# Performance work log

Measured on AMD Instinct MI355X. Metric: run time of the kernel, lower is better.

The kernel has to match this reference:

```python
import jax, jax.numpy as jnp
import numpy as np

B = 2048      # env batch (graphs)
A = 8         # agents per graph (fully connected)
N = B * A     # total nodes
DIN = 192     # raw obs dim
HD = 256      # h_dim (base MLP)
MD = 256      # mem_dim (GRU)
GD = 128      # gnn_dim (per-head GATv2 out, concat=False -> head mean)
H = 4         # GAT heads
NA = 20       # n_actions
ED = 3        # edge_dim


def setup_inputs() -> dict:
    key = jax.random.key(0)
    ks = jax.random.split(key, 16)
    # fully-connected directed graph per group of A agents, no self loops
    s, d = np.meshgrid(np.arange(A), np.arange(A), indexing='ij')
    mask = s != d
    s = s[mask]; d = d[mask]                     # [A*(A-1)]
    off = (np.arange(B) * A)[:, None]
    src = (off + s[None, :]).reshape(-1)
    dst = (off + d[None, :]).reshape(-1)
    edge_index = jnp.asarray(np.stack([src, dst]), dtype=jnp.int32)  # [2, E]
    E = src.shape[0]
    p = lambda k, sh: jax.random.normal(ks[k], sh, jnp.float32) * 0.02
    return {
        'inputs': jax.random.normal(ks[0], (N, DIN), jnp.float32),
        'hidden_states': jax.random.normal(ks[1], (N, MD), jnp.float32) * 0.1,
        'edge_index': edge_index,
        'edge_attr': jax.random.uniform(ks[2], (E, ED), jnp.float32),
        # base MLP (2 layers: Linear+ReLU+LayerNorm)
        'W1': p(3, (DIN, HD)), 'b1': jnp.zeros(HD), 'g1': jnp.ones(HD), 'be1': jnp.zeros(HD),
        'W2': p(4, (HD, HD)),  'b2': jnp.zeros(HD), 'g2': jnp.ones(HD), 'be2': jnp.zeros(HD),
        # GRUCell
        'Wih': p(5, (3 * MD, HD)), 'Whh': p(6, (3 * MD, MD)),
        'bih': jnp.zeros(3 * MD), 'bhh': jnp.zeros(3 * MD),
        # GATv2Conv (edge_dim=3, heads=4, concat=False, residual)
        'Wl': p(7, (MD, H * GD)), 'bl': jnp.zeros(H * GD),
        'Wr': p(8, (MD, H * GD)), 'br': jnp.zeros(H * GD),
        'att': p(9, (H, GD)),
        'We': p(10, (ED, H * GD)),
        'Wres': p(11, (MD, GD)),
        'bg': jnp.zeros(GD),
        # head: LayerNorm + Linear
        'lng': jnp.ones(GD), 'lnb': jnp.zeros(GD),
        'Wout': p(12, (GD, NA)), 'bout': jnp.zeros(NA),
    }


def _ln(x, g, b):
    mu = jnp.mean(x, -1, keepdims=True)
    xc = x - mu
    v = jnp.mean(xc * xc, -1, keepdims=True)
    return xc * jax.lax.rsqrt(v + 1e-5) * g + b


def _fwd(inputs, hidden_states, edge_attr, edge_index,
         W1, b1, g1, be1, W2, b2, g2, be2,
         Wih, Whh, bih, bhh,
         Wl, bl, Wr, br, att, We, Wres, bg,
         lng, lnb, Wout, bout):
    src, dst = edge_index[0], edge_index[1]
    # ---- base MLP encode ----
    x = _ln(jax.nn.relu(inputs @ W1 + b1), g1, be1)
    x = _ln(jax.nn.relu(x @ W2 + b2), g2, be2)          # [N, HD]
    # ---- SimpleConv(aggr='mean', combine_root='self_loop') ----
    s = jax.ops.segment_sum(x[src], dst, num_segments=N) + x
    deg = jax.ops.segment_sum(jnp.ones(src.shape[0], x.dtype), dst, num_segments=N) + 1.0
    x = s / deg[:, None]                                 # [N, HD]
    # ---- GRUCell ----
    gi = x @ Wih.T + bih
    gh = hidden_states @ Whh.T + bhh
    ir, iz, inn = jnp.split(gi, 3, -1)
    hr, hz, hn = jnp.split(gh, 3, -1)
    r = jax.nn.sigmoid(ir + hr)
    z = jax.nn.sigmoid(iz + hz)
    n = jnp.tanh(inn + r * hn)
    h = (1.0 - z) * n + z * hidden_states                # [N, MD]
    # ---- GATv2Conv (add self loops, edge_attr fill='mean') ----
    loop = jnp.arange(N, dtype=src.dtype)
    sf = jnp.concatenate([src, loop])
    df = jnp.concatenate([dst, loop])
    ea = jnp.concatenate([edge_attr, jnp.broadcast_to(edge_attr.mean(0), (N, ED))], 0)
    xl = (h @ Wl + bl).reshape(N, H, GD)
    xr = (h @ Wr + br).reshape(N, H, GD)
    m = xl[sf] + xr[df] + (ea @ We).reshape(-1, H, GD)   # [Ef, H, GD]
    m = jnp.where(m > 0, m, 0.2 * m)                     # leaky_relu(0.2)
    logits = jnp.einsum('ehc,hc->eh', m, att)            # [Ef, H]
    mx = jax.ops.segment_max(logits, df, num_segments=N)
    ex = jnp.exp(logits - mx[df])
    den = jax.ops.segment_sum(ex, df, num_segments=N)
    alpha = ex / (den[df] + 1e-16)                       # segment softmax
    out = jax.ops.segment_sum(xl[sf] * alpha[..., None], df, num_segments=N)
    out = out.mean(1) + h @ Wres + bg                    # head mean + residual + bias
    zg = jax.nn.relu(out)                                # [N, GD]
    # ---- action head ----
    q = _ln(zg, lng, lnb) @ Wout + bout                  # [N, NA]
    return q, h


def reference(inputs, hidden_states, edge_index, edge_attr,
              W1, b1, g1, be1, W2, b2, g2, be2,
              Wih, Whh, bih, bhh,
              Wl, bl, Wr, br, att, We, Wres, bg,
              lng, lnb, Wout, bout):
    return _fwd(inputs, hidden_states, edge_attr, edge_index,
                W1, b1, g1, be1, W2, b2, g2, be2,
                Wih, Whh, bih, bhh,
                Wl, bl, Wr, br, att, We, Wres, bg,
                lng, lnb, Wout, bout)
```

## Files before the change

kernel.cpp:

```cpp
#include <hip/hip_runtime.h>
#include <hip/hip_bf16.h>

constexpr int NB  = 2048;
constexpr int AG  = 8;
constexpr int NN  = NB * AG;
constexpr int DIN = 192;
constexpr int HD  = 256;
constexpr int MD  = 256;
constexpr int GD  = 128;
constexpr int NA  = 20;
constexpr int NE  = NB * AG * (AG - 1);

typedef __attribute__((ext_vector_type(8))) short bfrag8;
typedef __attribute__((ext_vector_type(4))) short sfrag4;
typedef __attribute__((ext_vector_type(4))) float f32x4;

#define MFMA16(a, b, c) __builtin_amdgcn_mfma_f32_16x16x32_bf16((a), (b), (c), 0, 0, 0)

__device__ __forceinline__ float bf2f(__hip_bfloat16 x) { return __bfloat162float(x); }
__device__ __forceinline__ __hip_bfloat16 f2bf(float x) { return __float2bfloat16(x); }
__device__ __forceinline__ short f2bs(float x) {
    __hip_bfloat16 b = __float2bfloat16(x);
    return *reinterpret_cast<short*>(&b);
}
__device__ __forceinline__ bfrag8 ldf(const __hip_bfloat16* p) { return *(const bfrag8*)p; }
__device__ __forceinline__ bfrag8 ldf32(const float* p) {
    const f32x4 a = *(const f32x4*)p;
    const f32x4 b = *(const f32x4*)(p + 4);
    bfrag8 r;
    r[0] = f2bs(a[0]); r[1] = f2bs(a[1]); r[2] = f2bs(a[2]); r[3] = f2bs(a[3]);
    r[4] = f2bs(b[0]); r[5] = f2bs(b[1]); r[6] = f2bs(b[2]); r[7] = f2bs(b[3]);
    return r;
}
__device__ __forceinline__ float sigmf(float x) { return 1.f / (1.f + __expf(-x)); }
__device__ __forceinline__ float blo(unsigned u) { return __uint_as_float(u << 16); }
__device__ __forceinline__ float bhi(unsigned u) { return __uint_as_float(u & 0xffff0000u); }

__global__ __launch_bounds__(256) void k_prep(
    const float* __restrict__ W1, const float* __restrict__ W2,
    const float* __restrict__ Wih, const float* __restrict__ Whh,
    const float* __restrict__ Wl, const float* __restrict__ bl,
    const float* __restrict__ Wr, const float* __restrict__ br,
    const float* __restrict__ Wres, const float* __restrict__ Wout,
    const float* __restrict__ ea,
    __hip_bfloat16* __restrict__ W1T, __hip_bfloat16* __restrict__ W2T,
    __hip_bfloat16* __restrict__ WihB, __hip_bfloat16* __restrict__ WhhB,
    __hip_bfloat16* __restrict__ WcatT, float* __restrict__ WoutTf,
    float* __restrict__ bcat, float* __restrict__ ea_partials)
{
    __shared__ float sw[4][3];
    const int tid = threadIdx.x;
    if (blockIdx.x >= 3151) {
        const int b = blockIdx.x - 3151;
        float a0 = 0.f, a1 = 0.f, a2 = 0.f;
#pragma unroll
        for (int k = 0; k < 7; k++) {
            int e = b * 1792 + k * 256 + tid;
            a0 += ea[e * 3 + 0];
            a1 += ea[e * 3 + 1];
            a2 += ea[e * 3 + 2];
        }
#pragma unroll
        for (int off = 1; off < 64; off <<= 1) {
            a0 += __shfl_xor(a0, off); a1 += __shfl_xor(a1, off); a2 += __shfl_xor(a2, off);
        }
        if ((tid & 63) == 0) { sw[tid >> 6][0] = a0; sw[tid >> 6][1] = a1; sw[tid >> 6][2] = a2; }
        __syncthreads();
        if (tid == 0) {
            ea_partials[b * 3 + 0] = sw[0][0] + sw[1][0] + sw[2][0] + sw[3][0];
            ea_partials[b * 3 + 1] = sw[0][1] + sw[1][1] + sw[2][1] + sw[3][1];
            ea_partials[b * 3 + 2] = sw[0][2] + sw[1][2] + sw[2][2] + sw[3][2];
        }
        return;
    }
    int i = blockIdx.x * 256 + tid;
    if (i < 49152) { int o = i / 192, c = i % 192; W1T[i] = f2bf(W1[c * 256 + o]); return; }
    i -= 49152;
    if (i < 65536) { int o = i >> 8, c = i & 255; W2T[i] = f2bf(W2[c * 256 + o]); return; }
    i -= 65536;
    if (i < 196608) { WihB[i] = f2bf(Wih[i]); return; }
    i -= 196608;
    if (i < 196608) { WhhB[i] = f2bf(Whh[i]); return; }
    i -= 196608;
    if (i < 294912) {
        int o = i >> 8, c = i & 255;
        float v;
        if (o < 512)       v = Wl[c * 512 + o];
        else if (o < 1024) v = Wr[c * 512 + (o - 512)];
        else               v = Wres[c * 128 + (o - 1024)];
        WcatT[i] = f2bf(v); return;
    }
    i -= 294912;
    if (i < 2560) { int o = i >> 7, c = i & 127; WoutTf[i] = Wout[c * 20 + o]; return; }
    i -= 2560;
    if (i < 1152) {
        float v = 0.f;
        if (i < 512) v = bl[i]; else if (i < 1024) v = br[i - 512];
        bcat[i] = v;
    }
}

__global__ __launch_bounds__(256) void k_encode(
    const float* __restrict__ in,
    const __hip_bfloat16* __restrict__ W1T,
    const float* __restrict__ b1, const float* __restrict__ g1, const float* __restrict__ be1,
    const __hip_bfloat16* __restrict__ W2T,
    const float* __restrict__ b2, const float* __restrict__ g2, const float* __restrict__ be2,
    __hip_bfloat16* __restrict__ xm)
{
    __shared__ float sf[16][257];
    __shared__ alignas(16) __hip_bfloat16 sb[16][264];
    const int tid = threadIdx.x;
    const int lane = tid & 63, w = tid >> 6;
    const int r = lane & 15, q = lane >> 4;
    const int m0 = blockIdx.x * 16;

    {
        bfrag8 af[6];
        const float* ap = in + (size_t)(m0 + r) * DIN + q * 8;
#pragma unroll
        for (int kb = 0; kb < 6; kb++) af[kb] = ldf32(ap + kb * 32);
#pragma unroll
        for (int i = 0; i < 4; i++) {
            int t = w * 4 + i;
            const __hip_bfloat16* wp = W1T + (size_t)(t * 16 + r) * DIN + q * 8;
            bfrag8 bf[6];
#pragma unroll
            for (int kb = 0; kb < 6; kb++) bf[kb] = ldf(wp + kb * 32);
            f32x4 acc = (f32x4){0.f, 0.f, 0.f, 0.f};
#pragma unroll
            for (int kb = 0; kb < 6; kb++) acc = MFMA16(af[kb], bf[kb], acc);
            int col = t * 16 + r;
            float bias = b1[col];
#pragma unroll
            for (int reg = 0; reg < 4; reg++)
                sf[q * 4 + reg][col] = fmaxf(acc[reg] + bias, 0.f);
        }
    }
    __syncthreads();
    {
        int rowi = tid >> 4, c16 = tid & 15;
        float vals[16]; float s = 0.f, s2 = 0.f;
#pragma unroll
        for (int j = 0; j < 16; j++) { float v = sf[rowi][c16 + 16 * j]; vals[j] = v; s += v; s2 += v * v; }
#pragma unroll
        for (int off = 1; off < 16; off <<= 1) { s += __shfl_xor(s, off); s2 += __shfl_xor(s2, off); }
        float mean = s * (1.f / HD);
        float var = fmaxf(s2 * (1.f / HD) - mean * mean, 0.f);
        float rs = rsqrtf(var + 1e-5f);
#pragma unroll
        for (int j = 0; j < 16; j++) {
            int col = c16 + 16 * j;
            sb[rowi][col] = f2bf((vals[j] - mean) * rs * g1[col] + be1[col]);
        }
    }
    __syncthreads();

    {
        bfrag8 af[8];
        const __hip_bfloat16* ap = &sb[r][0];
#pragma unroll
        for (int kb = 0; kb < 8; kb++) af[kb] = ldf(ap + kb * 32 + q * 8);
        float outv[4][4];
#pragma unroll
        for (int i = 0; i < 4; i++) {
            int t = w * 4 + i;
            const __hip_bfloat16* wp = W2T + (size_t)(t * 16 + r) * HD + q * 8;
            bfrag8 bf[8];
#pragma unroll
            for (int kb = 0; kb < 8; kb++) bf[kb] = ldf(wp + kb * 32);
            f32x4 acc = (f32x4){0.f, 0.f, 0.f, 0.f};
#pragma unroll
            for (int kb = 0; kb < 8; kb++) acc = MFMA16(af[kb], bf[kb], acc);
#pragma unroll
            for (int reg = 0; reg < 4; reg++) outv[i][reg] = acc[reg];
        }
        __syncthreads();
#pragma unroll
        for (int i = 0; i < 4; i++) {
            int col = (w * 4 + i) * 16 + r;
            float bias = b2[col];
#pragma unroll
            for (int reg = 0; reg < 4; reg++)
                sf[q * 4 + reg][col] = fmaxf(outv[i][reg] + bias, 0.f);
        }
    }
    __syncthreads();
    {
        int rowi = tid >> 4, c16 = tid & 15;
        float vals[16]; float s = 0.f, s2 = 0.f;
#pragma unroll
        for (int j = 0; j < 16; j++) { float v = sf[rowi][c16 + 16 * j]; vals[j] = v; s += v; s2 += v * v; }
#pragma unroll
        for (int off = 1; off < 16; off <<= 1) { s += __shfl_xor(s, off); s2 += __shfl_xor(s2, off); }
        float mean = s * (1.f / HD);
        float var = fmaxf(s2 * (1.f / HD) - mean * mean, 0.f);
        float rs = rsqrtf(var + 1e-5f);
#pragma unroll
        for (int j = 0; j < 16; j++) {
            int col = c16 + 16 * j;
            sb[rowi][col] = f2bf((vals[j] - mean) * rs * g2[col] + be2[col]);
        }
    }
    __syncthreads();
    {
        int col = tid;
        float a0 = 0.f, a1 = 0.f;
#pragma unroll
        for (int i = 0; i < 8; i++) { a0 += bf2f(sb[i][col]); a1 += bf2f(sb[8 + i][col]); }
        xm[(size_t)(2 * blockIdx.x) * HD + col] = f2bf(a0 * 0.125f);
        xm[(size_t)(2 * blockIdx.x + 1) * HD + col] = f2bf(a1 * 0.125f);
    }
}

__global__ __launch_bounds__(256, 2) void k_gruG(
    const float* __restrict__ hprev,
    const __hip_bfloat16* __restrict__ WhhB,
    const float* __restrict__ bhh,
    const __hip_bfloat16* __restrict__ xm,
    const __hip_bfloat16* __restrict__ WihB,
    const float* __restrict__ bih,
    float* __restrict__ hout)
{
    __shared__ alignas(16) float sgi[16][200];
    const int tid = threadIdx.x;
    const int lane = tid & 63, w = tid >> 6;
    const int r = lane & 15, q = lane >> 4;
    const int bswz = (blockIdx.x & 7) * 64 + (blockIdx.x >> 3);
    const int m0 = (bswz >> 2) * 128;
    const int cg = (bswz & 3) * 64;

    {
        const int g0 = m0 >> 3;
        bfrag8 axm[8];
        const __hip_bfloat16* ap = xm + (size_t)(g0 + r) * MD + q * 8;
#pragma unroll
        for (int kb = 0; kb < 8; kb++) axm[kb] = ldf(ap + kb * 32);
#pragma unroll
        for (int i = 0; i < 3; i++) {
            const int n = w * 3 + i;
            const int gate = n >> 2, nj = n & 3;
            const int colG = gate * 256 + cg + nj * 16 + r;
            const __hip_bfloat16* wp = WihB + (size_t)colG * MD + q * 8;
            bfrag8 bf[8];
#pragma unroll
            for (int kb = 0; kb < 8; kb++) bf[kb] = ldf(wp + kb * 32);
            f32x4 acg = (f32x4){0.f, 0.f, 0.f, 0.f};
#pragma unroll
            for (int kb = 0; kb < 8; kb++) acg = MFMA16(axm[kb], bf[kb], acg);
            const float bias = bih[colG];
#pragma unroll
            for (int reg = 0; reg < 4; reg++)
                sgi[q * 4 + reg][n * 16 + r] = acg[reg] + bias;
        }
    }

    bfrag8 afr[2][8];
#pragma unroll
    for (int t = 0; t < 2; t++) {
        const float* ap = hprev + (size_t)(m0 + (w * 2 + t) * 16 + r) * MD + q * 8;
#pragma unroll
        for (int kb = 0; kb < 8; kb++) afr[t][kb] = ldf32(ap + kb * 32);
    }
    __syncthreads();

    f32x4 acc[2][12];
#pragma unroll
    for (int t = 0; t < 2; t++)
#pragma unroll
        for (int n = 0; n < 12; n++) acc[t][n] = (f32x4){0.f, 0.f, 0.f, 0.f};

#pragma unroll
    for (int kb = 0; kb < 8; kb++) {
        bfrag8 bfB[12];
#pragma unroll
        for (int g = 0; g < 3; g++)
#pragma unroll
            for (int nj = 0; nj < 4; nj++)
                bfB[g * 4 + nj] = ldf(WhhB + (size_t)(g * 256 + cg + nj * 16 + r) * MD
                                      + kb * 32 + q * 8);
#pragma unroll
        for (int t = 0; t < 2; t++)
#pragma unroll
            for (int n = 0; n < 12; n++)
                acc[t][n] = MFMA16(bfB[n], afr[t][kb], acc[t][n]);
    }

#pragma unroll
    for (int t = 0; t < 2; t++) {
        int node = m0 + (w * 2 + t) * 16 + r;
        int gl = ((w * 2 + t) * 16 + r) >> 3;
#pragma unroll
        for (int nj = 0; nj < 4; nj++) {
            int c = cg + nj * 16 + q * 4;
            int ci = nj * 16 + q * 4;
            f32x4 gR = *(const f32x4*)&sgi[gl][ci];
            f32x4 gZ = *(const f32x4*)&sgi[gl][64 + ci];
            f32x4 gN = *(const f32x4*)&sgi[gl][128 + ci];
            f32x4 bR = *(const f32x4*)&bhh[c];
            f32x4 bZ = *(const f32x4*)&bhh[256 + c];
            f32x4 bN = *(const f32x4*)&bhh[512 + c];
            f32x4 hp = *(const f32x4*)&hprev[(size_t)node * MD + c];
            f32x4 hv;
#pragma unroll
            for (int reg = 0; reg < 4; reg++) {
                float rr = sigmf(gR[reg] + acc[t][0 + nj][reg] + bR[reg]);
                float zz = sigmf(gZ[reg] + acc[t][4 + nj][reg] + bZ[reg]);
                float nn = tanhf(gN[reg] + rr * (acc[t][8 + nj][reg] + bN[reg]));
                hv[reg] = (1.f - zz) * nn + zz * hp[reg];
            }
            *(f32x4*)&hout[(size_t)node * MD + c] = hv;
        }
    }
}

__global__ __launch_bounds__(64, 4) void k_xlr(
    const float* __restrict__ h,
    const __hip_bfloat16* __restrict__ WcatT,
    const float* __restrict__ bcat,
    __hip_bfloat16* __restrict__ xlr)
{
    const int lane = threadIdx.x;
    const int r = lane & 15, q = lane >> 4;

    const int lin = ((int)blockIdx.x & 7) * 576 + ((int)blockIdx.x >> 3);
    const int m0 = (lin / 18) * 64;
    const int nb = (lin % 18) * 64;

    const float* hbase = h + (size_t)(m0 + r) * MD + q * 8;
    const __hip_bfloat16* wbase = WcatT + (size_t)(nb + r) * MD + q * 8;

    f32x4 acc[4][4];
#pragma unroll
    for (int am = 0; am < 4; am++)
#pragma unroll
        for (int bn = 0; bn < 4; bn++) acc[am][bn] = (f32x4){0.f, 0.f, 0.f, 0.f};

#pragma unroll
    for (int kb = 0; kb < 8; ++kb) {
        bfrag8 af[4], bf[4];
#pragma unroll
        for (int am = 0; am < 4; ++am)
            af[am] = ldf32(hbase + (size_t)(am * 16) * MD + kb * 32);
#pragma unroll
        for (int bn = 0; bn < 4; ++bn)
            bf[bn] = ldf(wbase + (size_t)(bn * 16) * MD + kb * 32);
#pragma unroll
        for (int am = 0; am < 4; ++am)
#pragma unroll
            for (int bn = 0; bn < 4; ++bn)
                acc[am][bn] = MFMA16(bf[bn], af[am], acc[am][bn]);
    }

#pragma unroll
    for (int bn = 0; bn < 4; ++bn) {
        const int fb = nb + bn * 16 + q * 4;
        const f32x4 bv = *(const f32x4*)&bcat[fb];
#pragma unroll
        for (int am = 0; am < 4; ++am) {
            const int node = m0 + am * 16 + r;
            sfrag4 pk;
#pragma unroll
            for (int reg = 0; reg < 4; reg++) pk[reg] = f2bs(acc[am][bn][reg] + bv[reg]);
            *(sfrag4*)&xlr[(size_t)node * 1152 + fb] = pk;
        }
    }
}

__global__ __launch_bounds__(128, 4) void k_gat(
    const __hip_bfloat16* __restrict__ xlr,
    const float* __restrict__ ea,
    const float* __restrict__ ea_partials,
    const float* __restrict__ att,
    const float* __restrict__ We,
    const float* __restrict__ bg,
    const float* __restrict__ lng, const float* __restrict__ lnb,
    const float* __restrict__ WoutTf,
    const float* __restrict__ bout,
    float* __restrict__ qout)
{
    __shared__ alignas(16) char smem_raw[8 * 1160 * 2];
    __shared__ float slog[4][8][8];
    __shared__ float smean[4];
    __hip_bfloat16 (*sx)[1160] = (__hip_bfloat16 (*)[1160])smem_raw;
    float (*szg)[136] = (float (*)[136])smem_raw;
    const int tid = threadIdx.x;
    const int lane = tid & 63, w = tid >> 6;
    const int g = blockIdx.x;
    const int m0 = g * 8;

    if (tid < 3) {
        float s = 0.f;
        for (int i = 0; i < 64; i++) s += ea_partials[i * 3 + tid];
        smean[tid] = s * (1.f / NE);
    }
#pragma unroll
    for (int k = 0; k < 9; k++) {
        int idx = tid + k * 128;
        int row = idx / 144, off = (idx % 144) * 8;
        *(uint4*)&sx[row][off] = *(const uint4*)&xlr[(size_t)(m0 + row) * 1152 + off];
    }

    const int sL = lane & 7, dL = lane >> 3;
    float e0 = 0.f, e1 = 0.f, e2 = 0.f;
    if (sL != dL) {
        int eidx = sL * 7 + dL - (dL > sL ? 1 : 0);
        const float* ep = ea + (size_t)(g * 56 + eidx) * 3;
        e0 = ep[0]; e1 = ep[1]; e2 = ep[2];
    }
    __syncthreads();
    if (sL == dL) { e0 = smean[0]; e1 = smean[1]; e2 = smean[2]; }

    {
        const __hip_bfloat16* xlrow = &sx[sL][0];
        const __hip_bfloat16* xrrow = &sx[dL][512];
#pragma unroll
        for (int t = 0; t < 2; t++) {
            const int hh = w * 2 + t;
            const int woff = __builtin_amdgcn_readfirstlane(hh * 128);
            const float* attp = att + woff;
            const float* w0p = We + woff;
            const float* w1p = We + 512 + woff;
            const float* w2p = We + 1024 + woff;
            const __hip_bfloat16* xlp = xlrow + hh * 128;
            const __hip_bfloat16* xrp = xrrow + hh * 128;
            float p0 = 0.f, p1 = 0.f;
#pragma unroll 4
            for (int cb = 0; cb < 16; cb++) {
                const uint4 uxl = *(const uint4*)&xlp[cb * 8];
                const uint4 uxr = *(const uint4*)&xrp[cb * 8];
                const f32x4 a0  = *(const f32x4*)&attp[cb * 8];
                const f32x4 a1  = *(const f32x4*)&attp[cb * 8 + 4];
                const f32x4 w00 = *(const f32x4*)&w0p[cb * 8];
                const f32x4 w01 = *(const f32x4*)&w0p[cb * 8 + 4];
                const f32x4 w10 = *(const f32x4*)&w1p[cb * 8];
                const f32x4 w11 = *(const f32x4*)&w1p[cb * 8 + 4];
                const f32x4 w20 = *(const f32x4*)&w2p[cb * 8];
                const f32x4 w21 = *(const f32x4*)&w2p[cb * 8 + 4];
                float mm;
#define CH1(XL, XR, WA, WB, WC, AT, ACC)                                          \
                mm = fmaf(e2, (WC), fmaf(e1, (WB), fmaf(e0, (WA), (XL)))) + (XR); \
                mm = fmaxf(mm, 0.2f * mm); ACC = fmaf(mm, (AT), ACC);
                CH1(blo(uxl.x), blo(uxr.x), w00[0], w10[0], w20[0], a0[0], p0)
                CH1(bhi(uxl.x), bhi(uxr.x), w00[1], w10[1], w20[1], a0[1], p1)
                CH1(blo(uxl.y), blo(uxr.y), w00[2], w10[2], w20[2], a0[2], p0)
                CH1(bhi(uxl.y), bhi(uxr.y), w00[3], w10[3], w20[3], a0[3], p1)
                CH1(blo(uxl.z), blo(uxr.z), w01[0], w11[0], w21[0], a1[0], p0)
                CH1(bhi(uxl.z), bhi(uxr.z), w01[1], w11[1], w21[1], a1[1], p1)
                CH1(blo(uxl.w), blo(uxr.w), w01[2], w11[2], w21[2], a1[2], p0)
                CH1(bhi(uxl.w), bhi(uxr.w), w01[3], w11[3], w21[3], a1[3], p1)
#undef CH1
            }
            float p = p0 + p1;
            float mx = fmaxf(p, __shfl_xor(p, 1));
            mx = fmaxf(mx, __shfl_xor(mx, 2));
            mx = fmaxf(mx, __shfl_xor(mx, 4));
            float exv = __expf(p - mx);
            float den = exv + __shfl_xor(exv, 1);
            den += __shfl_xor(den, 2);
            den += __shfl_xor(den, 4);
            ((float*)&slog[hh][0][0])[lane] = exv / (den + 1e-16f);
        }
    }
    __syncthreads();

    {
        const int d = tid >> 4, cb = (tid & 15) * 8;
        float out[8] = {0.f, 0.f, 0.f, 0.f, 0.f, 0.f, 0.f, 0.f};
#pragma unroll
        for (int h = 0; h < 4; h++) {
#pragma unroll
            for (int s = 0; s < 8; s++) {
                const float al = slog[h][d][s];
                const uint4 u = *(const uint4*)&sx[s][h * 128 + cb];
                out[0] = fmaf(al, blo(u.x), out[0]);
                out[1] = fmaf(al, bhi(u.x), out[1]);
                out[2] = fmaf(al, blo(u.y), out[2]);
                out[3] = fmaf(al, bhi(u.y), out[3]);
                out[4] = fmaf(al, blo(u.z), out[4]);
                out[5] = fmaf(al, bhi(u.z), out[5]);
                out[6] = fmaf(al, blo(u.w), out[6]);
                out[7] = fmaf(al, bhi(u.w), out[7]);
            }
        }
        const uint4 ur = *(const uint4*)&sx[d][1024 + cb];
        const f32x4 bg0 = *(const f32x4*)&bg[cb];
        const f32x4 bg1 = *(const f32x4*)&bg[cb + 4];
        f32x4 ov0, ov1;
        ov0[0] = fmaxf(out[0] * 0.25f + blo(ur.x) + bg0[0], 0.f);
        ov0[1] = fmaxf(out[1] * 0.25f + bhi(ur.x) + bg0[1], 0.f);
        ov0[2] = fmaxf(out[2] * 0.25f + blo(ur.y) + bg0[2], 0.f);
        ov0[3] = fmaxf(out[3] * 0.25f + bhi(ur.y) + bg0[3], 0.f);
        ov1[0] = fmaxf(out[4] * 0.25f + blo(ur.z) + bg1[0], 0.f);
        ov1[1] = fmaxf(out[5] * 0.25f + bhi(ur.z) + bg1[1], 0.f);
        ov1[2] = fmaxf(out[6] * 0.25f + blo(ur.w) + bg1[2], 0.f);
        ov1[3] = fmaxf(out[7] * 0.25f + bhi(ur.w) + bg1[3], 0.f);
        __syncthreads();
        *(f32x4*)&szg[d][cb]     = ov0;
        *(f32x4*)&szg[d][cb + 4] = ov1;
    }
    __syncthreads();

    {
        int row = tid >> 4, j = tid & 15;
        float v[8]; float s = 0.f, s2 = 0.f;
#pragma unroll
        for (int cj = 0; cj < 8; cj++) { v[cj] = szg[row][j + 16 * cj]; s += v[cj]; s2 += v[cj] * v[cj]; }
#pragma unroll
        for (int off = 1; off < 16; off <<= 1) { s += __shfl_xor(s, off); s2 += __shfl_xor(s2, off); }
        float mean = s * (1.f / GD);
        float var = fmaxf(s2 * (1.f / GD) - mean * mean, 0.f);
        float rs = rsqrtf(var + 1e-5f);
#pragma unroll
        for (int cj = 0; cj < 8; cj++) {
            int c = j + 16 * cj;
            szg[row][c] = (v[cj] - mean) * rs * lng[c] + lnb[c];
        }
    }
    __syncthreads();

    {
        int row = tid >> 4, j = tid & 15;
        for (int jj = j; jj < NA; jj += 16) {
            float a = bout[jj];
            const float* wo = WoutTf + jj * 128;
#pragma unroll
            for (int c4 = 0; c4 < 32; c4++) {
                f32x4 z = *(const f32x4*)&szg[row][c4 * 4];
                const f32x4 wv = *(const f32x4*)&wo[c4 * 4];
                a = fmaf(z[0], wv[0], a); a = fmaf(z[1], wv[1], a);
                a = fmaf(z[2], wv[2], a); a = fmaf(z[3], wv[3], a);
            }
            qout[(size_t)(m0 + row) * NA + jj] = a;
        }
    }
}

extern "C" void kernel_launch(void* const* d_in, const int* in_sizes, int n_in,
                              void* d_out, int out_size, void* d_ws, size_t ws_size,
                              hipStream_t stream) {
    const float* inp   = (const float*)d_in[0];
    const float* hid   = (const float*)d_in[1];
    const float* eatt  = (const float*)d_in[3];
    const float* W1    = (const float*)d_in[4];
    const float* b1    = (const float*)d_in[5];
    const float* g1    = (const float*)d_in[6];
    const float* be1   = (const float*)d_in[7];
    const float* W2    = (const float*)d_in[8];
    const float* b2    = (const float*)d_in[9];
    const float* g2    = (const float*)d_in[10];
    const float* be2   = (const float*)d_in[11];
    const float* Wih   = (const float*)d_in[12];
    const float* Whh   = (const float*)d_in[13];
    const float* bih   = (const float*)d_in[14];
    const float* bhh   = (const float*)d_in[15];
    const float* Wl    = (const float*)d_in[16];
    const float* bl    = (const float*)d_in[17];
    const float* Wr    = (const float*)d_in[18];
    const float* br    = (const float*)d_in[19];
    const float* att   = (const float*)d_in[20];
    const float* We    = (const float*)d_in[21];
    const float* Wres  = (const float*)d_in[22];
    const float* bg    = (const float*)d_in[23];
    const float* lng   = (const float*)d_in[24];
    const float* lnb   = (const float*)d_in[25];
    const float* Wout  = (const float*)d_in[26];
    const float* bout  = (const float*)d_in[27];

    float* qout = (float*)d_out;
    float* hout = (float*)d_out + (size_t)NN * NA;

    char* ws = (char*)d_ws;
    float*           ea_partials = (float*)ws;
    __hip_bfloat16*  xm    = (__hip_bfloat16*)(ws + 2048);
    __hip_bfloat16*  W1T   = (__hip_bfloat16*)(ws + 7342080);
    __hip_bfloat16*  W2T   = (__hip_bfloat16*)(ws + 7440384);
    __hip_bfloat16*  WihB  = (__hip_bfloat16*)(ws + 7571456);
    __hip_bfloat16*  WhhB  = (__hip_bfloat16*)(ws + 7964672);
    __hip_bfloat16*  WcatT = (__hip_bfloat16*)(ws + 8357888);
    float*           bcat  = (float*)(ws + 8947712);
    float*           WoutTf= (float*)(ws + 8952320);
    __hip_bfloat16*  xlr   = (__hip_bfloat16*)(ws + 8962560);

    k_prep<<<3215, 256, 0, stream>>>(W1, W2, Wih, Whh, Wl, bl, Wr, br, Wres, Wout, eatt,
                                     W1T, W2T, WihB, WhhB, WcatT, WoutTf, bcat, ea_partials);
    k_encode<<<NN / 16, 256, 0, stream>>>(inp, W1T, b1, g1, be1, W2T, b2, g2, be2, xm);
    k_gruG<<<512, 256, 0, stream>>>(hid, WhhB, bhh, xm, WihB, bih, hout);
    k_xlr<<<4608, 64, 0, stream>>>(hout, WcatT, bcat, xlr);
    k_gat<<<NB, 128, 0, stream>>>(xlr, eatt, ea_partials, att, We, bg,
                                  lng, lnb, WoutTf, bout, qout);
}
```

Baseline: 320.8 us.

## Fuse xl/xr/res projection GEMM into GAT kernel, processing two graphs per block

```diff
diff --git a/kernel.cpp b/kernel.cpp
--- a/kernel.cpp
+++ b/kernel.cpp
@@ -314,61 +314,10 @@
     }
 }
 
-__global__ __launch_bounds__(64, 4) void k_xlr(
+__global__ __launch_bounds__(256, 4) void k_gat(
     const float* __restrict__ h,
     const __hip_bfloat16* __restrict__ WcatT,
     const float* __restrict__ bcat,
-    __hip_bfloat16* __restrict__ xlr)
-{
-    const int lane = threadIdx.x;
-    const int r = lane & 15, q = lane >> 4;
-
-    const int lin = ((int)blockIdx.x & 7) * 576 + ((int)blockIdx.x >> 3);
-    const int m0 = (lin / 18) * 64;
-    const int nb = (lin % 18) * 64;
-
-    const float* hbase = h + (size_t)(m0 + r) * MD + q * 8;
-    const __hip_bfloat16* wbase = WcatT + (size_t)(nb + r) * MD + q * 8;
-
-    f32x4 acc[4][4];
-#pragma unroll
-    for (int am = 0; am < 4; am++)
-#pragma unroll
-        for (int bn = 0; bn < 4; bn++) acc[am][bn] = (f32x4){0.f, 0.f, 0.f, 0.f};
-
-#pragma unroll
-    for (int kb = 0; kb < 8; ++kb) {
-        bfrag8 af[4], bf[4];
-#pragma unroll
-        for (int am = 0; am < 4; ++am)
-            af[am] = ldf32(hbase + (size_t)(am * 16) * MD + kb * 32);
-#pragma unroll
-        for (int bn = 0; bn < 4; ++bn)
-            bf[bn] = ldf(wbase + (size_t)(bn * 16) * MD + kb * 32);
-#pragma unroll
-        for (int am = 0; am < 4; ++am)
-#pragma unroll
-            for (int bn = 0; bn < 4; ++bn)
-                acc[am][bn] = MFMA16(bf[bn], af[am], acc[am][bn]);
-    }
-
-#pragma unroll
-    for (int bn = 0; bn < 4; ++bn) {
-        const int fb = nb + bn * 16 + q * 4;
-        const f32x4 bv = *(const f32x4*)&bcat[fb];
-#pragma unroll
-        for (int am = 0; am < 4; ++am) {
-            const int node = m0 + am * 16 + r;
-            sfrag4 pk;
-#pragma unroll
-            for (int reg = 0; reg < 4; reg++) pk[reg] = f2bs(acc[am][bn][reg] + bv[reg]);
-            *(sfrag4*)&xlr[(size_t)node * 1152 + fb] = pk;
-        }
-    }
-}
-
-__global__ __launch_bounds__(128, 4) void k_gat(
-    const __hip_bfloat16* __restrict__ xlr,
     const float* __restrict__ ea,
     const float* __restrict__ ea_partials,
     const float* __restrict__ att,
@@ -379,44 +328,62 @@
     const float* __restrict__ bout,
     float* __restrict__ qout)
 {
-    __shared__ alignas(16) char smem_raw[8 * 1160 * 2];
-    __shared__ float slog[4][8][8];
+    __shared__ alignas(16) char smem_raw[16 * 1160 * 2];
+    __shared__ float slog[2][4][8][8];
     __shared__ float smean[4];
     __hip_bfloat16 (*sx)[1160] = (__hip_bfloat16 (*)[1160])smem_raw;
     float (*szg)[136] = (float (*)[136])smem_raw;
     const int tid = threadIdx.x;
     const int lane = tid & 63, w = tid >> 6;
-    const int g = blockIdx.x;
-    const int m0 = g * 8;
+    const int m0 = blockIdx.x * 16;
 
     if (tid < 3) {
         float s = 0.f;
         for (int i = 0; i < 64; i++) s += ea_partials[i * 3 + tid];
         smean[tid] = s * (1.f / NE);
     }
-#pragma unroll
-    for (int k = 0; k < 9; k++) {
-        int idx = tid + k * 128;
-        int row = idx / 144, off = (idx % 144) * 8;
-        *(uint4*)&sx[row][off] = *(const uint4*)&xlr[(size_t)(m0 + row) * 1152 + off];
-    }
-
+
+    const int r = lane & 15, q = lane >> 4;
     const int sL = lane & 7, dL = lane >> 3;
+    const int gg = w >> 1;
     float e0 = 0.f, e1 = 0.f, e2 = 0.f;
     if (sL != dL) {
         int eidx = sL * 7 + dL - (dL > sL ? 1 : 0);
-        const float* ep = ea + (size_t)(g * 56 + eidx) * 3;
+        const float* ep = ea + (size_t)((blockIdx.x * 2 + gg) * 56 + eidx) * 3;
         e0 = ep[0]; e1 = ep[1]; e2 = ep[2];
     }
+
+    {
+        bfrag8 af[8];
+        const float* ap = h + (size_t)(m0 + r) * MD + q * 8;
+#pragma unroll
+        for (int kb = 0; kb < 8; kb++) af[kb] = ldf32(ap + kb * 32);
+#pragma unroll
+        for (int i = 0; i < 18; i++) {
+            const int t = i * 4 + w;
+            const __hip_bfloat16* wp = WcatT + (size_t)(t * 16 + r) * MD + q * 8;
+            bfrag8 bf[8];
+#pragma unroll
+            for (int kb = 0; kb < 8; kb++) bf[kb] = ldf(wp + kb * 32);
+            f32x4 acc = (f32x4){0.f, 0.f, 0.f, 0.f};
+#pragma unroll
+            for (int kb = 0; kb < 8; kb++) acc = MFMA16(af[kb], bf[kb], acc);
+            const int col = t * 16 + r;
+            const float bias = bcat[col];
+#pragma unroll
+            for (int reg = 0; reg < 4; reg++)
+                sx[q * 4 + reg][col] = f2bf(acc[reg] + bias);
+        }
+    }
     __syncthreads();
     if (sL == dL) { e0 = smean[0]; e1 = smean[1]; e2 = smean[2]; }
 
     {
-        const __hip_bfloat16* xlrow = &sx[sL][0];
-        const __hip_bfloat16* xrrow = &sx[dL][512];
+        const __hip_bfloat16* xlrow = &sx[gg * 8 + sL][0];
+        const __hip_bfloat16* xrrow = &sx[gg * 8 + dL][512];
 #pragma unroll
         for (int t = 0; t < 2; t++) {
-            const int hh = w * 2 + t;
+            const int hh = (w & 1) * 2 + t;
             const int woff = __builtin_amdgcn_readfirstlane(hh * 128);
             const float* attp = att + woff;
             const float* w0p = We + woff;
@@ -459,20 +426,21 @@
             float den = exv + __shfl_xor(exv, 1);
             den += __shfl_xor(den, 2);
             den += __shfl_xor(den, 4);
-            ((float*)&slog[hh][0][0])[lane] = exv / (den + 1e-16f);
-        }
-    }
-    __syncthreads();
-
-    {
-        const int d = tid >> 4, cb = (tid & 15) * 8;
+            ((float*)&slog[gg][hh][0][0])[lane] = exv / (den + 1e-16f);
+        }
+    }
+    __syncthreads();
+
+    {
+        const int d16 = tid >> 4, cb = (tid & 15) * 8;
+        const int ag = d16 >> 3, dd = d16 & 7;
         float out[8] = {0.f, 0.f, 0.f, 0.f, 0.f, 0.f, 0.f, 0.f};
 #pragma unroll
-        for (int h = 0; h < 4; h++) {
+        for (int hh = 0; hh < 4; hh++) {
 #pragma unroll
             for (int s = 0; s < 8; s++) {
-                const float al = slog[h][d][s];
-                const uint4 u = *(const uint4*)&sx[s][h * 128 + cb];
+                const float al = slog[ag][hh][dd][s];
+                const uint4 u = *(const uint4*)&sx[ag * 8 + s][hh * 128 + cb];
                 out[0] = fmaf(al, blo(u.x), out[0]);
                 out[1] = fmaf(al, bhi(u.x), out[1]);
                 out[2] = fmaf(al, blo(u.y), out[2]);
@@ -483,7 +451,7 @@
                 out[7] = fmaf(al, bhi(u.w), out[7]);
             }
         }
-        const uint4 ur = *(const uint4*)&sx[d][1024 + cb];
+        const uint4 ur = *(const uint4*)&sx[d16][1024 + cb];
         const f32x4 bg0 = *(const f32x4*)&bg[cb];
         const f32x4 bg1 = *(const f32x4*)&bg[cb + 4];
         f32x4 ov0, ov1;
@@ -496,8 +464,8 @@
         ov1[2] = fmaxf(out[6] * 0.25f + blo(ur.w) + bg1[2], 0.f);
         ov1[3] = fmaxf(out[7] * 0.25f + bhi(ur.w) + bg1[3], 0.f);
         __syncthreads();
-        *(f32x4*)&szg[d][cb]     = ov0;
-        *(f32x4*)&szg[d][cb + 4] = ov1;
+        *(f32x4*)&szg[d16][cb]     = ov0;
+        *(f32x4*)&szg[d16][cb + 4] = ov1;
     }
     __syncthreads();
 
@@ -580,13 +548,11 @@
     __hip_bfloat16*  WcatT = (__hip_bfloat16*)(ws + 8357888);
     float*           bcat  = (float*)(ws + 8947712);
     float*           WoutTf= (float*)(ws + 8952320);
-    __hip_bfloat16*  xlr   = (__hip_bfloat16*)(ws + 8962560);
 
     k_prep<<<3215, 256, 0, stream>>>(W1, W2, Wih, Whh, Wl, bl, Wr, br, Wres, Wout, eatt,
                                      W1T, W2T, WihB, WhhB, WcatT, WoutTf, bcat, ea_partials);
     k_encode<<<NN / 16, 256, 0, stream>>>(inp, W1T, b1, g1, be1, W2T, b2, g2, be2, xm);
     k_gruG<<<512, 256, 0, stream>>>(hid, WhhB, bhh, xm, WihB, bih, hout);
-    k_xlr<<<4608, 64, 0, stream>>>(hout, WcatT, bcat, xlr);
-    k_gat<<<NB, 128, 0, stream>>>(xlr, eatt, ea_partials, att, We, bg,
-                                  lng, lnb, WoutTf, bout, qout);
-}
+    k_gat<<<NB / 2, 256, 0, stream>>>(hout, WcatT, bcat, eatt, ea_partials, att, We, bg,
+                                      lng, lnb, WoutTf, bout, qout);
+}
```

Measured after the change: 312.6 us. 2.6% less time.
